# Kernel tuning notes

Hardware: AMD Instinct MI355X
Metric: run time of the kernel (lower is better)

The kernel has to match this reference:

```python
import jax, jax.numpy as jnp
import numpy as np


def setup_inputs() -> dict:
    key = jax.random.key(0)
    k1, k2 = jax.random.split(key)
    N, P, SMK, L = 256, 64, 2048, 32
    inp = jax.random.normal(k1, (N, P, SMK, 2), dtype=jnp.float32)
    # channel taps; in the original these are randn scaled by sqrt(power/2)
    cof = jax.random.normal(k2, (N, P, L, 2), dtype=jnp.float32) * 0.1
    return {"input": inp, "cof": cof, "M": 64}


def reference(input, cof, M):
    # input: (N, P, SMK, 2) real/imag stacked; cof: (N, P, L, 2)
    N, P, SMK, _ = input.shape
    L = cof.shape[2]
    sig = (input[..., 0] + 1j * input[..., 1]).reshape(N * P, SMK)   # complex64
    h = (cof[..., 0] + 1j * cof[..., 1]).reshape(N * P, L)
    # torch path: conv1d with time-reversed taps and padding=L-1 == FULL linear
    # convolution; four real convs == one complex conv.
    out_c = jax.vmap(lambda s, k: jnp.convolve(s, k, mode="full"))(sig, h)  # (N*P, SMK+L-1)
    output = jnp.stack([out_c.real, out_c.imag], axis=-1).reshape(N, P, SMK + L - 1, 2)
    # H_t = FFT of zero-padded taps along the tap axis (length M)
    cof_zp = jnp.pad(cof, ((0, 0), (0, 0), (0, M - L), (0, 0)))
    Hc = jnp.fft.fft(cof_zp[..., 0] + 1j * cof_zp[..., 1], axis=-1)  # (N, P, M)
    H_t = jnp.stack([Hc.real, Hc.imag], axis=-1)                      # (N, P, M, 2)
    return output, H_t
```

## Files before the change

### kernel.cpp

```cpp
#include <hip/hip_runtime.h>
#include <math.h>

#define SMK    2048
#define TAPS   32
#define OUTLEN (SMK + TAPS - 1)
#define PAD    32
#define SLOTS  (PAD + SMK + PAD)
#define NF4    (SLOTS / 2)
#define MDFT   64

typedef float v2f __attribute__((ext_vector_type(2)));

__device__ __forceinline__ float rfl(float x) {
    return __int_as_float(__builtin_amdgcn_readfirstlane(__float_as_int(x)));
}

__global__ __launch_bounds__(256, 8)
void conv_kernel(const float* __restrict__ input,
                 const float* __restrict__ cof,
                 float* __restrict__ out0,
                 float* __restrict__ out1)
{
    __shared__ float4 S4[NF4];
    __shared__ float2 s_tw[MDFT];

    const int tid = threadIdx.x;
    const int row = blockIdx.x;

    const float4* gin = (const float4*)(input + (size_t)row * (SMK * 2));
    #pragma unroll
    for (int k = 0; k < 4; ++k) S4[16 + tid + 256 * k] = gin[tid + 256 * k];
    if (tid < 16) {
        S4[tid] = make_float4(0.f, 0.f, 0.f, 0.f);
    } else if (tid < 32) {
        S4[1024 + tid] = make_float4(0.f, 0.f, 0.f, 0.f);
    }
    if (tid >= 64 && tid < 128) {
        int j = tid - 64;
        float sv, cv;
        __sincosf(-2.0f * (float)M_PI * (float)j / (float)MDFT, &sv, &cv);
        s_tw[j] = make_float2(cv, sv);
    }

    const float2* __restrict__ ct = (const float2*)(cof + (size_t)row * (TAPS * 2));
    float hre[TAPS], him[TAPS];
    #pragma unroll
    for (int l = 0; l < TAPS; ++l) {
        float2 tv = ct[l];
        hre[l] = rfl(tv.x);
        him[l] = rfl(tv.y);
    }
    __syncthreads();

    float2* go2 = (float2*)(out0 + (size_t)row * (OUTLEN * 2));

    #pragma unroll 1
    for (int j = 0; j < 4; ++j) {
        const int t0 = 2 * tid + 1 + 512 * j;

        v2f accA[2], accB[2];
        #pragma unroll
        for (int k = 0; k < 2; ++k) { accA[k] = (v2f)(0.f); accB[k] = (v2f)(0.f); }

        #pragma unroll
        for (int c = 0; c < 4; ++c) {
            const int base4 = tid + 13 + 256 * j - 4 * c;
            float4 w4[5];
            #pragma unroll
            for (int i = 0; i < 5; ++i) w4[i] = S4[base4 + i];

            #pragma unroll
            for (int lp = 0; lp < 8; ++lp) {
                const int l = 8 * c + lp;
                const v2f hv = { hre[l], him[l] };
                #pragma unroll
                for (int k = 0; k < 2; ++k) {
                    const int m = k - lp + 7;
                    const float sx = (m & 1) ? w4[m >> 1].z : w4[m >> 1].x;
                    const float sy = (m & 1) ? w4[m >> 1].w : w4[m >> 1].y;
                    accA[k] = __builtin_elementwise_fma((v2f){ sx, sx }, hv, accA[k]);
                    accB[k] = __builtin_elementwise_fma((v2f){ sy, sy }, hv, accB[k]);
                }
            }
            __builtin_amdgcn_sched_barrier(0);
        }

        go2[t0]     = make_float2(accA[0].x - accB[0].y, accA[0].y + accB[0].x);
        go2[t0 + 1] = make_float2(accA[1].x - accB[1].y, accA[1].y + accB[1].x);
    }

    const float2* S2 = (const float2*)S4;

    if (tid < MDFT) {
        const int kk = tid;
        v2f aA = (v2f)(0.f), aB = (v2f)(0.f);
        #pragma unroll
        for (int l = 0; l < TAPS; ++l) {
            const v2f hv = { hre[l], him[l] };
            float2 w = s_tw[(kk * l) & (MDFT - 1)];
            aA = __builtin_elementwise_fma((v2f){ w.x, w.x }, hv, aA);
            aB = __builtin_elementwise_fma((v2f){ w.y, w.y }, hv, aB);
        }
        ((float2*)out1)[(size_t)row * MDFT + kk] =
            make_float2(aA.x - aB.y, aA.y + aB.x);
    }
    else if (tid >= 128 && tid <= 158) {
        const int t = (tid == 158) ? 0 : (2049 + (tid - 128));
        v2f aA = (v2f)(0.f), aB = (v2f)(0.f);
        #pragma unroll
        for (int l = 0; l < TAPS; ++l) {
            const v2f hv = { hre[l], him[l] };
            float2 s = S2[PAD + t - l];
            aA = __builtin_elementwise_fma((v2f){ s.x, s.x }, hv, aA);
            aB = __builtin_elementwise_fma((v2f){ s.y, s.y }, hv, aB);
        }
        go2[t] = make_float2(aA.x - aB.y, aA.y + aB.x);
    }
}

extern "C" void kernel_launch(void* const* d_in, const int* in_sizes, int n_in,
                              void* d_out, int out_size, void* d_ws, size_t ws_size,
                              hipStream_t stream)
{
    const float* input = (const float*)d_in[0];
    const float* cof   = (const float*)d_in[1];

    const int NP = in_sizes[0] / (SMK * 2);

    float* out0 = (float*)d_out;
    float* out1 = out0 + (size_t)NP * OUTLEN * 2;

    conv_kernel<<<NP, 256, 0, stream>>>(input, cof, out0, out1);
}
```

Before: 136.3 us.

## Make conv kernel persistent over 8 rows with register-staged prefetch of next row

Launches a fixed 2048 blocks that each process 8 rows in a strided loop, instead of one block per row. The next row's input and taps are loaded into registers and a double-buffered shared tap array while the current row is computed, so global load latency overlaps with the FMA work. The cost is extra registers for the staging buffer, which may lower occupancy. The grid size is hardcoded and assumes NP = 16384.

Result: slower. 222.2 us (+63.0%).

```diff
diff --git a/kernel.cpp b/kernel.cpp
--- a/kernel.cpp
+++ b/kernel.cpp
@@ -8,6 +8,8 @@
 #define SLOTS  (PAD + SMK + PAD)
 #define NF4    (SLOTS / 2)
 #define MDFT   64
+#define ROWS_PER_BLOCK 8
+#define NBLOCKS 2048
 
 typedef float v2f __attribute__((ext_vector_type(2)));
 
@@ -23,13 +25,10 @@
 {
     __shared__ float4 S4[NF4];
     __shared__ float2 s_tw[MDFT];
+    __shared__ float2 s_tap[2][TAPS];
 
     const int tid = threadIdx.x;
-    const int row = blockIdx.x;
 
-    const float4* gin = (const float4*)(input + (size_t)row * (SMK * 2));
-    #pragma unroll
-    for (int k = 0; k < 4; ++k) S4[16 + tid + 256 * k] = gin[tid + 256 * k];
     if (tid < 16) {
         S4[tid] = make_float4(0.f, 0.f, 0.f, 0.f);
     } else if (tid < 32) {
@@ -42,79 +41,107 @@
         s_tw[j] = make_float2(cv, sv);
     }
 
-    const float2* __restrict__ ct = (const float2*)(cof + (size_t)row * (TAPS * 2));
-    float hre[TAPS], him[TAPS];
-    #pragma unroll
-    for (int l = 0; l < TAPS; ++l) {
-        float2 tv = ct[l];
-        hre[l] = rfl(tv.x);
-        him[l] = rfl(tv.y);
+    float4 stg[4];
+    {
+        const float4* g = (const float4*)(input + (size_t)blockIdx.x * (SMK * 2));
+        #pragma unroll
+        for (int k = 0; k < 4; ++k) stg[k] = g[tid + 256 * k];
+        if (tid < TAPS) {
+            const float2* ct = (const float2*)(cof + (size_t)blockIdx.x * (TAPS * 2));
+            s_tap[0][tid] = ct[tid];
+        }
     }
-    __syncthreads();
-
-    float2* go2 = (float2*)(out0 + (size_t)row * (OUTLEN * 2));
 
     #pragma unroll 1
-    for (int j = 0; j < 4; ++j) {
-        const int t0 = 2 * tid + 1 + 512 * j;
+    for (int it = 0; it < ROWS_PER_BLOCK; ++it) {
+        const size_t r = (size_t)blockIdx.x + (size_t)NBLOCKS * it;
 
-        v2f accA[2], accB[2];
+        __syncthreads();
         #pragma unroll
-        for (int k = 0; k < 2; ++k) { accA[k] = (v2f)(0.f); accB[k] = (v2f)(0.f); }
+        for (int k = 0; k < 4; ++k) S4[16 + tid + 256 * k] = stg[k];
+        __syncthreads();
 
+        float hre[TAPS], him[TAPS];
         #pragma unroll
-        for (int c = 0; c < 4; ++c) {
-            const int base4 = tid + 13 + 256 * j - 4 * c;
-            float4 w4[5];
+        for (int l = 0; l < TAPS; ++l) {
+            float2 tv = s_tap[it & 1][l];
+            hre[l] = rfl(tv.x);
+            him[l] = rfl(tv.y);
+        }
+
+        if (it + 1 < ROWS_PER_BLOCK) {
+            const float4* gn = (const float4*)(input + (r + NBLOCKS) * (size_t)(SMK * 2));
             #pragma unroll
-            for (int i = 0; i < 5; ++i) w4[i] = S4[base4 + i];
+            for (int k = 0; k < 4; ++k) stg[k] = gn[tid + 256 * k];
+            if (tid < TAPS) {
+                const float2* ctn = (const float2*)(cof + (r + NBLOCKS) * (size_t)(TAPS * 2));
+                s_tap[(it + 1) & 1][tid] = ctn[tid];
+            }
+        }
+
+        float2* go2 = (float2*)(out0 + r * (size_t)(OUTLEN * 2));
+
+        #pragma unroll 1
+        for (int j = 0; j < 4; ++j) {
+            const int t0 = 2 * tid + 1 + 512 * j;
+
+            v2f accA[2], accB[2];
+            #pragma unroll
+            for (int k = 0; k < 2; ++k) { accA[k] = (v2f)(0.f); accB[k] = (v2f)(0.f); }
 
             #pragma unroll
-            for (int lp = 0; lp < 8; ++lp) {
-                const int l = 8 * c + lp;
-                const v2f hv = { hre[l], him[l] };
+            for (int c = 0; c < 4; ++c) {
+                const int base4 = tid + 13 + 256 * j - 4 * c;
+                float4 w4[5];
                 #pragma unroll
-                for (int k = 0; k < 2; ++k) {
-                    const int m = k - lp + 7;
-                    const float sx = (m & 1) ? w4[m >> 1].z : w4[m >> 1].x;
-                    const float sy = (m & 1) ? w4[m >> 1].w : w4[m >> 1].y;
-                    accA[k] = __builtin_elementwise_fma((v2f){ sx, sx }, hv, accA[k]);
-                    accB[k] = __builtin_elementwise_fma((v2f){ sy, sy }, hv, accB[k]);
+                for (int i = 0; i < 5; ++i) w4[i] = S4[base4 + i];
+
+                #pragma unroll
+                for (int lp = 0; lp < 8; ++lp) {
+                    const int l = 8 * c + lp;
+                    const v2f hv = { hre[l], him[l] };
+                    #pragma unroll
+                    for (int k = 0; k < 2; ++k) {
+                        const int m = k - lp + 7;
+                        const float sx = (m & 1) ? w4[m >> 1].z : w4[m >> 1].x;
+                        const float sy = (m & 1) ? w4[m >> 1].w : w4[m >> 1].y;
+                        accA[k] = __builtin_elementwise_fma((v2f){ sx, sx }, hv, accA[k]);
+                        accB[k] = __builtin_elementwise_fma((v2f){ sy, sy }, hv, accB[k]);
+                    }
                 }
+                __builtin_amdgcn_sched_barrier(0);
             }
-            __builtin_amdgcn_sched_barrier(0);
+
+            go2[t0]     = make_float2(accA[0].x - accB[0].y, accA[0].y + accB[0].x);
+            go2[t0 + 1] = make_float2(accA[1].x - accB[1].y, accA[1].y + accB[1].x);
         }
 
-        go2[t0]     = make_float2(accA[0].x - accB[0].y, accA[0].y + accB[0].x);
-        go2[t0 + 1] = make_float2(accA[1].x - accB[1].y, accA[1].y + accB[1].x);
-    }
+        const float2* S2 = (const float2*)S4;
 
-    const float2* S2 = (const float2*)S4;
-
-    if (tid < MDFT) {
-        const int kk = tid;
-        v2f aA = (v2f)(0.f), aB = (v2f)(0.f);
-        #pragma unroll
-        for (int l = 0; l < TAPS; ++l) {
-            const v2f hv = { hre[l], him[l] };
-            float2 w = s_tw[(kk * l) & (MDFT - 1)];
-            aA = __builtin_elementwise_fma((v2f){ w.x, w.x }, hv, aA);
-            aB = __builtin_elementwise_fma((v2f){ w.y, w.y }, hv, aB);
+        if (tid < MDFT) {
+            const int kk = tid;
+            v2f aA = (v2f)(0.f), aB = (v2f)(0.f);
+            #pragma unroll
+            for (int l = 0; l < TAPS; ++l) {
+                const v2f hv = { hre[l], him[l] };
+                float2 w = s_tw[(kk * l) & (MDFT - 1)];
+                aA = __builtin_elementwise_fma((v2f){ w.x, w.x }, hv, aA);
+                aB = __builtin_elementwise_fma((v2f){ w.y, w.y }, hv, aB);
+            }
+            ((float2*)out1)[r * MDFT + kk] = make_float2(aA.x - aB.y, aA.y + aB.x);
         }
-        ((float2*)out1)[(size_t)row * MDFT + kk] =
-            make_float2(aA.x - aB.y, aA.y + aB.x);
-    }
-    else if (tid >= 128 && tid <= 158) {
-        const int t = (tid == 158) ? 0 : (2049 + (tid - 128));
-        v2f aA = (v2f)(0.f), aB = (v2f)(0.f);
-        #pragma unroll
-        for (int l = 0; l < TAPS; ++l) {
-            const v2f hv = { hre[l], him[l] };
-            float2 s = S2[PAD + t - l];
-            aA = __builtin_elementwise_fma((v2f){ s.x, s.x }, hv, aA);
-            aB = __builtin_elementwise_fma((v2f){ s.y, s.y }, hv, aB);
+        else if (tid >= 128 && tid <= 158) {
+            const int t = (tid == 158) ? 0 : (2049 + (tid - 128));
+            v2f aA = (v2f)(0.f), aB = (v2f)(0.f);
+            #pragma unroll
+            for (int l = 0; l < TAPS; ++l) {
+                const v2f hv = { hre[l], him[l] };
+                float2 s = S2[PAD + t - l];
+                aA = __builtin_elementwise_fma((v2f){ s.x, s.x }, hv, aA);
+                aB = __builtin_elementwise_fma((v2f){ s.y, s.y }, hv, aB);
+            }
+            go2[t] = make_float2(aA.x - aB.y, aA.y + aB.x);
         }
-        go2[t] = make_float2(aA.x - aB.y, aA.y + aB.x);
     }
 }
 
@@ -125,10 +152,9 @@
     const float* input = (const float*)d_in[0];
     const float* cof   = (const float*)d_in[1];
 
+    float* out0 = (float*)d_out;
     const int NP = in_sizes[0] / (SMK * 2);
-
-    float* out0 = (float*)d_out;
     float* out1 = out0 + (size_t)NP * OUTLEN * 2;
 
-    conv_kernel<<<NP, 256, 0, stream>>>(input, cof, out0, out1);
+    conv_kernel<<<NBLOCKS, 256, 0, stream>>>(input, cof, out0, out1);
 }
```
